# Optimization experiments

Measured on AMD Instinct MI355X. Metric: run time of the kernel, lower is better.

## Reference

```python
import jax, jax.numpy as jnp
import numpy as np

B, N, C, H = 2, 2048, 1024, 16
D = C // H
SCALE = D ** -0.5


def setup_inputs() -> dict:
    key = jax.random.key(0)
    ks = jax.random.split(key, 5)
    x = jax.random.normal(ks[0], (B, N, C), dtype=jnp.float32)
    # causal mask, broadcast over batch: True = attend
    attention_mask = jnp.broadcast_to(jnp.tril(jnp.ones((N, N), dtype=bool)), (B, N, N))
    w_qkv = jax.random.normal(ks[1], (3 * C, C), dtype=jnp.float32) * (C ** -0.5)
    b_qkv = jax.random.normal(ks[2], (3 * C,), dtype=jnp.float32) * 0.02
    w_proj = jax.random.normal(ks[3], (C, C), dtype=jnp.float32) * (C ** -0.5)
    b_proj = jax.random.normal(ks[4], (C,), dtype=jnp.float32) * 0.02
    return {"x": x, "attention_mask": attention_mask, "w_qkv": w_qkv,
            "b_qkv": b_qkv, "w_proj": w_proj, "b_proj": b_proj}


def reference(x, attention_mask, w_qkv, b_qkv, w_proj, b_proj):
    b, n, c = x.shape
    qkv = x @ w_qkv.T + b_qkv                      # [B,N,3C]
    qkv = qkv.reshape(b, n, 3, H, D).transpose(2, 0, 3, 1, 4)  # [3,B,H,N,D]
    q, k, v = qkv[0], qkv[1], qkv[2]
    dots = jnp.einsum('bhid,bhjd->bhij', q, k) * SCALE
    mask_value = -jnp.finfo(dots.dtype).max
    dots = jnp.where(attention_mask[:, None, :, :], dots, mask_value)
    attn = jax.nn.softmax(dots.astype(jnp.float32), axis=-1).astype(dots.dtype)
    out = jnp.einsum('bhij,bhjd->bhid', attn, v)   # [B,H,N,D]
    # NOTE: original code reshapes WITHOUT transposing heads back - faithful.
    out = out.reshape(b, n, c)
    return out @ w_proj.T + b_proj
```

## Files before the change

### kernel.cpp

```cpp
#include <hip/hip_runtime.h>
#include <hip/hip_bf16.h>
#include <stdint.h>

#define SL_F 0.18033688011112043f

typedef unsigned short u16;
typedef unsigned int u32;
typedef __attribute__((ext_vector_type(8))) short bf16x8;
typedef __attribute__((ext_vector_type(4))) float f32x4;

__device__ __forceinline__ u16 f2bf(float f) {
    union { float f; u32 u; } v; v.f = f;
    return (u16)((v.u + 0x7fffu + ((v.u >> 16) & 1u)) >> 16);
}
__device__ __forceinline__ u32 pack2bf(float a, float b) {
    union { __hip_bfloat162 h; u32 u; } p;
    p.h = __float22bfloat162_rn(make_float2(a, b));
    return p.u;
}

__device__ __forceinline__ void gl_lds16(const u16* g, u16* l) {
    __builtin_amdgcn_global_load_lds(
        (const __attribute__((address_space(1))) u32*)g,
        (__attribute__((address_space(3))) u32*)l, 16, 0, 0);
}

__global__ __launch_bounds__(256) void convert_k(
    const float* __restrict__ x, const float* __restrict__ w1,
    const float* __restrict__ w2,
    u16* __restrict__ xb, u16* __restrict__ w1b, u16* __restrict__ w2b)
{
    const int t = blockIdx.x * 256 + threadIdx.x;
    const int XA = 524288, XW1 = 393216;
    const float* src; u16* dst; int s;
    if (t < XA)            { src = x;  dst = xb;  s = t; }
    else if (t < XA + XW1) { src = w1; dst = w1b; s = t - XA; }
    else                   { src = w2; dst = w2b; s = t - XA - XW1; }
    const int c = s >> 6;
    const int u = s & 63;
    const int l = (u >> 2) + 16 * (u & 3);
    const int g = c >> 5, kb = c & 31;
    const int row = g * 16 + (l & 15);
    const int k0 = kb * 32 + (l >> 4) * 8;
    const float4 v0 = *(const float4*)&src[(size_t)row * 1024 + k0];
    const float4 v1 = *(const float4*)&src[(size_t)row * 1024 + k0 + 4];
    uint4 o;
    o.x = pack2bf(v0.x, v0.y); o.y = pack2bf(v0.z, v0.w);
    o.z = pack2bf(v1.x, v1.y); o.w = pack2bf(v1.z, v1.w);
    *(uint4*)&dst[((size_t)c * 64 + l) * 8] = o;
}

__global__ __launch_bounds__(256) void qkv_gemm(
    const u16* __restrict__ A, const u16* __restrict__ Bw,
    const float* __restrict__ bias,
    u16* __restrict__ Qb, u16* __restrict__ Kb, u16* __restrict__ VTb)
{
    __shared__ __align__(16) u16 Al[2][8 * 512];
    __shared__ __align__(16) u16 Bl[2][8 * 512];
    const int tid = threadIdx.x;
    const int lane = tid & 63;
    const int w = tid >> 6;
    const int la = lane & 15, qd = lane >> 4;
    const int m0 = blockIdx.y * 128;
    const int n0 = blockIdx.x * 128;
    const int wm = (w >> 1) * 64, wn = (w & 1) * 64;

    const u16* Ag0 = A + ((size_t)((m0 >> 4) + 2 * w) * 32) * 512 + lane * 8;
    const u16* Ag1 = Ag0 + 32 * 512;
    const u16* Bg0 = Bw + ((size_t)((n0 >> 4) + 2 * w) * 32) * 512 + lane * 8;
    const u16* Bg1 = Bg0 + 32 * 512;

    auto stage = [&](int k0, int b) {
        const size_t ko = (size_t)(k0 >> 5) * 512;
        gl_lds16(Ag0 + ko, &Al[b][(2 * w) * 512]);
        gl_lds16(Ag1 + ko, &Al[b][(2 * w + 1) * 512]);
        gl_lds16(Bg0 + ko, &Bl[b][(2 * w) * 512]);
        gl_lds16(Bg1 + ko, &Bl[b][(2 * w + 1) * 512]);
    };

    f32x4 acc[4][4] = {};
    int buf = 0;
    stage(0, 0);

    for (int k0 = 0; k0 < 1024; k0 += 32) {
        __syncthreads();
        if (k0 + 32 < 1024) stage(k0 + 32, buf ^ 1);

        bf16x8 af[4], bfr[4];
#pragma unroll
        for (int i = 0; i < 4; i++)
            af[i] = *(const bf16x8*)&Al[buf][(((unsigned)wm >> 4) + i) * 512 + lane * 8];
#pragma unroll
        for (int j = 0; j < 4; j++)
            bfr[j] = *(const bf16x8*)&Bl[buf][(((unsigned)wn >> 4) + j) * 512 + lane * 8];
#pragma unroll
        for (int i = 0; i < 4; i++)
#pragma unroll
            for (int j = 0; j < 4; j++)
                acc[i][j] = __builtin_amdgcn_mfma_f32_16x16x32_bf16(
                    af[i], bfr[j], acc[i][j], 0, 0, 0);
        buf ^= 1;
    }

#pragma unroll
    for (int j = 0; j < 4; j++) {
        const int col = n0 + wn + j * 16 + la;
        const float bv = bias[col];
        const int t = col >> 10, hd = col & 1023, h = hd >> 6, d = hd & 63;
#pragma unroll
        for (int i = 0; i < 4; i++)
#pragma unroll
            for (int r = 0; r < 4; r++) {
                const int row = m0 + wm + i * 16 + qd * 4 + r;
                const int b = row >> 11, n = row & 2047;
                const int bh = b * 16 + h;
                const u16 val = f2bf(acc[i][j][r] + bv);
                if (t == 0)
                    Qb[((size_t)bh * 2048 + n) * 64 + d] = val;
                else if (t == 1)
                    Kb[((size_t)bh * 256 + (n >> 4) * 2 + (d >> 5)) * 512
                       + ((n & 15) + 16 * ((d >> 3) & 3)) * 8 + (d & 7)] = val;
                else
                    VTb[((size_t)bh * 256 + (n >> 7) * 16 + (d >> 4) * 4 + ((n >> 5) & 3)) * 512
                        + ((d & 15) + 16 * ((n >> 3) & 3)) * 8 + (n & 7)] = val;
            }
    }
}

__global__ __launch_bounds__(256) void proj_gemm(
    const u16* __restrict__ A, const u16* __restrict__ Bw,
    const float* __restrict__ bias, float* __restrict__ Out)
{
    __shared__ __align__(16) u16 Al[2][16 * 512];
    __shared__ __align__(16) u16 Bl[2][8 * 512];
    const int tid = threadIdx.x;
    const int lane = tid & 63;
    const int w = tid >> 6;
    const int la = lane & 15, qd = lane >> 4;
    const int K = 1024;
    const int m0 = blockIdx.y * 128;
    const int n0 = blockIdx.x * 64;
    const int wm = (w >> 1) * 64, wn = (w & 1) * 32;

    const u16* Ab[4];
#pragma unroll
    for (int t = 0; t < 4; t++) {
        const int ck = 4 * w + t, g = ck >> 1, h = ck & 1;
        Ab[t] = A + (((size_t)(m0 >> 4) + g) * 32 + h) * 512 + lane * 8;
    }
    const u16* Bg = Bw + ((size_t)((n0 >> 4) + w) * 32) * 512 + lane * 8;

    auto stage = [&](int k0, int b) {
#pragma unroll
        for (int t = 0; t < 4; t++)
            gl_lds16(Ab[t] + (size_t)(k0 >> 5) * 512, &Al[b][(4 * w + t) * 512]);
#pragma unroll
        for (int t = 0; t < 2; t++)
            gl_lds16(Bg + (size_t)((k0 >> 5) + t) * 512, &Bl[b][(2 * w + t) * 512]);
    };

    f32x4 acc[4][2] = {};
    int buf = 0;
    stage(0, 0);

    for (int k0 = 0; k0 < K; k0 += 64) {
        __syncthreads();
        if (k0 + 64 < K) stage(k0 + 64, buf ^ 1);

        bf16x8 af[4][2], bfr[2][2];
#pragma unroll
        for (int i = 0; i < 4; i++) {
            const int g = ((unsigned)wm >> 4) + i;
#pragma unroll
            for (int h = 0; h < 2; h++)
                af[i][h] = *(const bf16x8*)&Al[buf][(g * 2 + h) * 512 + lane * 8];
        }
#pragma unroll
        for (int j = 0; j < 2; j++) {
            const int g = ((unsigned)wn >> 4) + j;
#pragma unroll
            for (int h = 0; h < 2; h++)
                bfr[j][h] = *(const bf16x8*)&Bl[buf][(g * 2 + h) * 512 + lane * 8];
        }
#pragma unroll
        for (int i = 0; i < 4; i++)
#pragma unroll
            for (int j = 0; j < 2; j++) {
                f32x4 c = acc[i][j];
                c = __builtin_amdgcn_mfma_f32_16x16x32_bf16(af[i][0], bfr[j][0], c, 0, 0, 0);
                c = __builtin_amdgcn_mfma_f32_16x16x32_bf16(af[i][1], bfr[j][1], c, 0, 0, 0);
                acc[i][j] = c;
            }
        buf ^= 1;
    }

#pragma unroll
    for (int j = 0; j < 2; j++) {
        const int col = n0 + wn + j * 16 + la;
        const float bv = bias[col];
#pragma unroll
        for (int i = 0; i < 4; i++)
#pragma unroll
            for (int r = 0; r < 4; r++) {
                const int row = m0 + wm + i * 16 + qd * 4 + r;
                Out[(size_t)row * 1024 + col] = acc[i][j][r] + bv;
            }
    }
}

__global__ __launch_bounds__(256) void attn_k(
    const u16* __restrict__ Qb, const u16* __restrict__ Kb,
    const u16* __restrict__ VTb, u16* __restrict__ Ob)
{
    __shared__ __align__(16) u16 Kl[2][16 * 512];
    __shared__ __align__(16) u16 Vl[2][16 * 512];
    __shared__ __align__(16) u16 Pl[4][16 * 72];
    const int bh = blockIdx.x & 31;
    const int pair = blockIdx.x >> 5;
    const int tid = threadIdx.x;
    const int lane = tid & 63;
    const int w = tid >> 6;
    const int la = lane & 15, qd = lane >> 4;

    const u16* Kbh = Kb + (size_t)bh * 256 * 512 + lane * 8;
    const u16* Vbh = VTb + (size_t)bh * 256 * 512 + lane * 8;
    u16* Pw = &Pl[w][0];

    auto stage = [&](int j0, int b) {
#pragma unroll
        for (int t = 0; t < 4; t++) {
            const int ck = 4 * w + t;
            gl_lds16(Kbh + (size_t)((j0 >> 3) + ck) * 512, &Kl[b][ck * 512]);
            gl_lds16(Vbh + (size_t)((j0 >> 7) * 16 + ck) * 512, &Vl[b][ck * 512]);
        }
    };

    int buf = 0;
    stage(0, 0);

    for (int half = 0; half < 2; half++) {
        const int tile = (half == 0) ? pair : 31 - pair;
        const int q0 = tile * 64 + w * 16;
        const int jmax = (tile >> 1) * 128;
        const int qrow = q0 + la;

        const u16* Qp = Qb + ((size_t)bh * 2048 + q0 + la) * 64 + qd * 8;
        const bf16x8 qf0 = *(const bf16x8*)Qp;
        const bf16x8 qf1 = *(const bf16x8*)(Qp + 32);

        f32x4 o[4] = {};
        float lsum = 0.f;

        for (int j0 = 0; j0 <= jmax; j0 += 128) {
            __syncthreads();

            const int nj = (j0 + 128 <= jmax) ? (j0 + 128) : ((half == 0) ? 0 : -1);
            if (nj >= 0) stage(nj, buf ^ 1);

            f32x4 s[8];
#pragma unroll
            for (int c = 0; c < 8; c++) {
                f32x4 z = {};
                const bf16x8 kf0 = *(const bf16x8*)&Kl[buf][(c * 2 + 0) * 512 + lane * 8];
                const bf16x8 kf1 = *(const bf16x8*)&Kl[buf][(c * 2 + 1) * 512 + lane * 8];
                z = __builtin_amdgcn_mfma_f32_16x16x32_bf16(kf0, qf0, z, 0, 0, 0);
                z = __builtin_amdgcn_mfma_f32_16x16x32_bf16(kf1, qf1, z, 0, 0, 0);
                s[c] = z;
            }

            if (j0 == jmax) {
#pragma unroll
                for (int c = 0; c < 8; c++)
#pragma unroll
                    for (int r = 0; r < 4; r++) {
                        const int j = j0 + c * 16 + qd * 4 + r;
                        float v = s[c][r] * SL_F;
                        v = (j > qrow) ? -1e30f : v;
                        s[c][r] = __builtin_amdgcn_exp2f(v);
                    }
            } else {
#pragma unroll
                for (int c = 0; c < 8; c++)
#pragma unroll
                    for (int r = 0; r < 4; r++)
                        s[c][r] = __builtin_amdgcn_exp2f(s[c][r] * SL_F);
            }
#pragma unroll
            for (int c = 0; c < 8; c++)
#pragma unroll
                for (int r = 0; r < 4; r++)
                    lsum += s[c][r];

#pragma unroll
            for (int hh = 0; hh < 2; hh++) {
#pragma unroll
                for (int c = 0; c < 4; c++) {
                    uint2 pw;
                    pw.x = pack2bf(s[hh * 4 + c][0], s[hh * 4 + c][1]);
                    pw.y = pack2bf(s[hh * 4 + c][2], s[hh * 4 + c][3]);
                    *(uint2*)&Pw[la * 72 + c * 16 + qd * 4] = pw;
                }
                const bf16x8 pf0 = *(const bf16x8*)&Pw[la * 72 + qd * 8];
                const bf16x8 pf1 = *(const bf16x8*)&Pw[la * 72 + 32 + qd * 8];
#pragma unroll
                for (int c2 = 0; c2 < 4; c2++) {
                    const bf16x8 vf0 = *(const bf16x8*)&Vl[buf][(c2 * 4 + hh * 2 + 0) * 512 + lane * 8];
                    const bf16x8 vf1 = *(const bf16x8*)&Vl[buf][(c2 * 4 + hh * 2 + 1) * 512 + lane * 8];
                    o[c2] = __builtin_amdgcn_mfma_f32_16x16x32_bf16(pf0, vf0, o[c2], 0, 0, 0);
                    o[c2] = __builtin_amdgcn_mfma_f32_16x16x32_bf16(pf1, vf1, o[c2], 0, 0, 0);
                }
            }
            buf ^= 1;
        }

        lsum += __shfl_xor(lsum, 16, 64);
        lsum += __shfl_xor(lsum, 32, 64);
        float rinv[4];
#pragma unroll
        for (int r = 0; r < 4; r++)
            rinv[r] = 1.0f / __shfl(lsum, qd * 4 + r, 64);

        const int m = bh * 128 + (q0 >> 4);
        u16* Ot = Ob + ((size_t)(m >> 4) * 32) * 512;
        const int mm = m & 15;
#pragma unroll
        for (int c2 = 0; c2 < 4; c2++)
#pragma unroll
            for (int r = 0; r < 4; r++) {
                const int kk5 = (qd * 4 + r) * 2 + (c2 >> 1);
                const int s3 = (c2 * 2 + (la >> 3)) & 3;
                Ot[(size_t)kk5 * 512 + (mm + 16 * s3) * 8 + (la & 7)] =
                    f2bf(o[c2][r] * rinv[r]);
            }
    }
}

extern "C" void kernel_launch(void* const* d_in, const int* in_sizes, int n_in,
                              void* d_out, int out_size, void* d_ws, size_t ws_size,
                              hipStream_t stream)
{
    const float* x     = (const float*)d_in[0];
    const float* wqkv  = (const float*)d_in[2];
    const float* bqkv  = (const float*)d_in[3];
    const float* wproj = (const float*)d_in[4];
    const float* bproj = (const float*)d_in[5];
    float* out = (float*)d_out;

    u16* ws     = (u16*)d_ws;
    u16* xb     = ws;
    u16* wqkvb  = xb + 4096 * 1024;
    u16* wprojb = wqkvb + 3072 * 1024;
    u16* Qb     = wprojb + 1024 * 1024;
    u16* Kb     = Qb + 32 * 2048 * 64;
    u16* VTb    = Kb + 32 * 2048 * 64;
    u16* Ob     = VTb + 32 * 2048 * 64;

    convert_k<<<dim3(4096), dim3(256), 0, stream>>>(
        x, wqkv, wproj, xb, wqkvb, wprojb);

    qkv_gemm<<<dim3(24, 32), dim3(256), 0, stream>>>(
        xb, wqkvb, bqkv, Qb, Kb, VTb);

    attn_k<<<dim3(512), dim3(256), 0, stream>>>(Qb, Kb, VTb, Ob);

    proj_gemm<<<dim3(16, 32), dim3(256), 0, stream>>>(
        Ob, wprojb, bproj, out);
}
```

Before: 212.1 us.

## Reorder K/V global layout so QKV epilogue writes contiguous runs

Changes the in-memory layout of the K and transposed-V buffers written by the QKV GEMM epilogue so that consecutive lanes/rows land at nearby addresses, and hoists per-type address computation out of the inner store loops. The attention kernel's staging loads are adjusted with a lane permutation and new V chunk indexing to read the new layout into the same LDS arrangement. The aim is fewer scattered 2-byte stores in the epilogue, at the cost of possibly less contiguous global_load_lds reads in attention.

After: 188.6 us. 11.1% less time.

```diff
diff --git a/kernel.cpp b/kernel.cpp
--- a/kernel.cpp
+++ b/kernel.cpp
@@ -102,28 +102,41 @@
         buf ^= 1;
     }
 
+    const int b_ = m0 >> 11;
+    const int nb = (m0 & 2047) + wm;
 #pragma unroll
     for (int j = 0; j < 4; j++) {
-        const int col = n0 + wn + j * 16 + la;
+        const int colb = n0 + wn + j * 16;
+        const int col = colb + la;
         const float bv = bias[col];
-        const int t = col >> 10, hd = col & 1023, h = hd >> 6, d = hd & 63;
-#pragma unroll
-        for (int i = 0; i < 4; i++)
-#pragma unroll
-            for (int r = 0; r < 4; r++) {
-                const int row = m0 + wm + i * 16 + qd * 4 + r;
-                const int b = row >> 11, n = row & 2047;
-                const int bh = b * 16 + h;
-                const u16 val = f2bf(acc[i][j][r] + bv);
-                if (t == 0)
-                    Qb[((size_t)bh * 2048 + n) * 64 + d] = val;
-                else if (t == 1)
-                    Kb[((size_t)bh * 256 + (n >> 4) * 2 + (d >> 5)) * 512
-                       + ((n & 15) + 16 * ((d >> 3) & 3)) * 8 + (d & 7)] = val;
-                else
-                    VTb[((size_t)bh * 256 + (n >> 7) * 16 + (d >> 4) * 4 + ((n >> 5) & 3)) * 512
-                        + ((d & 15) + 16 * ((n >> 3) & 3)) * 8 + (n & 7)] = val;
-            }
+        const int t = colb >> 10;
+        const int hd = col & 1023, h = hd >> 6, d = hd & 63;
+        const int bh = b_ * 16 + h;
+        if (t == 0) {
+            u16* QB = Qb + ((size_t)bh * 2048 + nb) * 64 + d;
+#pragma unroll
+            for (int i = 0; i < 4; i++)
+#pragma unroll
+                for (int r = 0; r < 4; r++)
+                    QB[(i * 16 + qd * 4 + r) * 64] = f2bf(acc[i][j][r] + bv);
+        } else if (t == 1) {
+            u16* KB = Kb + (size_t)bh * 131072
+                    + (size_t)((nb >> 4) * 2 + (d >> 5)) * 512 + (d & 31);
+#pragma unroll
+            for (int i = 0; i < 4; i++)
+#pragma unroll
+                for (int r = 0; r < 4; r++)
+                    KB[i * 1024 + (qd * 4 + r) * 32] = f2bf(acc[i][j][r] + bv);
+        } else {
+            u16* VB = VTb + (size_t)bh * 131072
+                    + (size_t)(d >> 4) * 32768 + (d & 15) * 32;
+#pragma unroll
+            for (int i = 0; i < 4; i++)
+#pragma unroll
+                for (int r = 0; r < 4; r++)
+                    VB[((nb >> 5) + (i >> 1)) * 512 + (i & 1) * 16 + qd * 4 + r]
+                        = f2bf(acc[i][j][r] + bv);
+        }
     }
 }
 
@@ -222,8 +235,9 @@
     const int w = tid >> 6;
     const int la = lane & 15, qd = lane >> 4;
 
-    const u16* Kbh = Kb + (size_t)bh * 256 * 512 + lane * 8;
-    const u16* Vbh = VTb + (size_t)bh * 256 * 512 + lane * 8;
+    const int perm = (lane & 15) * 32 + (lane >> 4) * 8;
+    const u16* Kbh = Kb + (size_t)bh * 131072 + perm;
+    const u16* Vbh = VTb + (size_t)bh * 131072 + perm;
     u16* Pw = &Pl[w][0];
 
     auto stage = [&](int j0, int b) {
@@ -231,7 +245,8 @@
         for (int t = 0; t < 4; t++) {
             const int ck = 4 * w + t;
             gl_lds16(Kbh + (size_t)((j0 >> 3) + ck) * 512, &Kl[b][ck * 512]);
-            gl_lds16(Vbh + (size_t)((j0 >> 7) * 16 + ck) * 512, &Vl[b][ck * 512]);
+            gl_lds16(Vbh + (size_t)((ck >> 2) * 64 + (j0 >> 5) + (ck & 3)) * 512,
+                     &Vl[b][ck * 512]);
         }
     };
 
```
